# Optimization experiments

Measured on AMD Instinct MI355X. Metric: run time of the kernel, lower is better.

## Reference

```python
import jax, jax.numpy as jnp
import numpy as np

N_NODES = 50000
N_EDGES = 600000
IN_DIM, HID, OUT_DIM = 128, 128, 64


def setup_inputs() -> dict:
    key = jax.random.key(0)
    ks = jax.random.split(key, 12)
    h = jax.random.normal(ks[0], (N_NODES, IN_DIM), dtype=jnp.float32)
    src = jax.random.randint(ks[1], (N_EDGES,), 0, N_NODES, dtype=jnp.int32)
    dst = jax.random.randint(ks[2], (N_EDGES,), 0, N_NODES, dtype=jnp.int32)
    dims = [(IN_DIM, HID), (HID, HID), (HID, HID), (HID, OUT_DIM)]
    params = {}
    for i, (di, do) in enumerate(dims):
        scale = 1.0 / np.sqrt(di)
        params[f"W{i}"] = jax.random.uniform(ks[3 + i], (di, do), jnp.float32, -scale, scale)
        params[f"b{i}"] = jnp.zeros((do,), jnp.float32)
    return dict(h=h, src=src, dst=dst, **params)


def _gcn_layer(h, W, b, src, dst, norm_src, norm_dst, n_nodes):
    # DGL GraphConv, norm='both': D^{-1/2} A D^{-1/2} (h W) + b
    x = (h * norm_src) @ W              # [N, out]
    agg = jax.ops.segment_sum(x[src], dst, num_segments=n_nodes)
    return agg * norm_dst + b


def reference(h, src, dst, W0, b0, W1, b1, W2, b2, W3, b3):
    n = h.shape[0]
    ones = jnp.ones((src.shape[0],), h.dtype)
    deg_out = jnp.clip(jax.ops.segment_sum(ones, src, num_segments=n), 1.0)
    deg_in = jnp.clip(jax.ops.segment_sum(ones, dst, num_segments=n), 1.0)
    norm_src = (deg_out ** -0.5)[:, None]
    norm_dst = (deg_in ** -0.5)[:, None]
    Ws = [(W0, b0), (W1, b1), (W2, b2), (W3, b3)]
    for i, (W, b) in enumerate(Ws):
        h = _gcn_layer(h, W, b, src, dst, norm_src, norm_dst, n)
        if i != len(Ws) - 1:
            h = jax.nn.relu(h)  # dropout is identity in eval mode
    return h
```

## Files before the change

### kernel.cpp

```cpp
#include <hip/hip_runtime.h>


namespace {

constexpr int NN = 50000;
constexpr int NE = 600000;
constexpr int SCAN_BLK = 256;
constexpr int NBLK = (NN + SCAN_BLK - 1) / SCAN_BLK;
constexpr int EB = (NE + 255) / 256;
constexpr int MFMA_BLOCKS = (NN / 16 + 3) / 4;
constexpr int WCVT_ELEMS = 16384 * 3 + 8192;
constexpr int WCVT_BLOCKS = WCVT_ELEMS / 256;

typedef unsigned short bhalf;
typedef __attribute__((ext_vector_type(8))) short short8v;
typedef __attribute__((ext_vector_type(4))) float f32x4;

__device__ inline float blo(unsigned int v) {
  return __uint_as_float(v << 16);
}
__device__ inline float bhi(unsigned int v) {
  return __uint_as_float(v & 0xFFFF0000u);
}
__device__ inline unsigned int f2b_bits(float f) {
  unsigned int b = __float_as_uint(f);
  return b + 0x7FFFu + ((b >> 16) & 1u);
}
__device__ inline unsigned int pack2(float lo, float hi) {
  return (f2b_bits(lo) >> 16) | (f2b_bits(hi) & 0xFFFF0000u);
}
__device__ inline bhalf f2b(float f) { return (bhalf)(f2b_bits(f) >> 16); }

__global__ __launch_bounds__(256) void wcvt_kernel(
    const float* __restrict__ W0, const float* __restrict__ W1,
    const float* __restrict__ W2, const float* __restrict__ W3,
    bhalf* __restrict__ wt0, bhalf* __restrict__ wt1,
    bhalf* __restrict__ wt2, bhalf* __restrict__ wt3) {
  int flat = blockIdx.x * 256 + threadIdx.x;
  if (flat < 16384) {
    int j = flat >> 7, k = flat & 127;
    wt0[flat] = f2b(W0[k * 128 + j]);
  } else if (flat < 32768) {
    int f = flat - 16384;
    int j = f >> 7, k = f & 127;
    wt1[f] = f2b(W1[k * 128 + j]);
  } else if (flat < 49152) {
    int f = flat - 32768;
    int j = f >> 7, k = f & 127;
    wt2[f] = f2b(W2[k * 128 + j]);
  } else {
    int f = flat - 49152;
    int j = f >> 7, k = f & 127;
    wt3[f] = f2b(W3[k * 64 + j]);
  }
}

__global__ void deg_loc_kernel(const int* __restrict__ src, const int* __restrict__ dst,
                               int* __restrict__ dego, int* __restrict__ degi,
                               int* __restrict__ le) {
  int e = blockIdx.x * blockDim.x + threadIdx.x;
  if (e < NE) {
    atomicAdd(&dego[src[e]], 1);
    le[e] = atomicAdd(&degi[dst[e]], 1);
  }
}

__global__ __launch_bounds__(SCAN_BLK) void scan1_norm(const int* __restrict__ dego,
                                                       const int* __restrict__ degi,
                                                       int* __restrict__ bsum,
                                                       float* __restrict__ ns,
                                                       float* __restrict__ nd) {
  __shared__ int ws[SCAN_BLK / 64];
  int i = blockIdx.x * SCAN_BLK + threadIdx.x;
  int v = 0;
  if (i < NN) {
    int din = degi[i];
    int dout = dego[i];
    v = din;
    int a = dout < 1 ? 1 : dout;
    int b = din < 1 ? 1 : din;
    ns[i] = 1.0f / sqrtf((float)a);
    nd[i] = 1.0f / sqrtf((float)b);
  }
#pragma unroll
  for (int off = 32; off; off >>= 1) v += __shfl_down(v, off, 64);
  int lane = threadIdx.x & 63, w = threadIdx.x >> 6;
  if (lane == 0) ws[w] = v;
  __syncthreads();
  if (threadIdx.x == 0) {
    int s = 0;
#pragma unroll
    for (int k = 0; k < SCAN_BLK / 64; ++k) s += ws[k];
    bsum[blockIdx.x] = s;
  }
}

__global__ __launch_bounds__(SCAN_BLK) void scan23(const int* __restrict__ deg,
                                                   const int* __restrict__ bsum,
                                                   int* __restrict__ rowptr) {
  __shared__ int sb[SCAN_BLK];
  __shared__ int s[SCAN_BLK];
  const int t = threadIdx.x;
  int vb = (t < NBLK) ? bsum[t] : 0;
  sb[t] = vb;
  __syncthreads();
  for (int off = 1; off < SCAN_BLK; off <<= 1) {
    int u = (t >= off) ? sb[t - off] : 0;
    __syncthreads();
    sb[t] += u;
    __syncthreads();
  }
  const int pre = (blockIdx.x == 0) ? 0 : sb[blockIdx.x - 1];
  if (blockIdx.x == NBLK - 1 && t == 0) rowptr[NN] = sb[NBLK - 1];

  int i = blockIdx.x * SCAN_BLK + t;
  int v = (i < NN) ? deg[i] : 0;
  s[t] = v;
  __syncthreads();
  for (int off = 1; off < SCAN_BLK; off <<= 1) {
    int u = (t >= off) ? s[t - off] : 0;
    __syncthreads();
    s[t] += u;
    __syncthreads();
  }
  if (i < NN) rowptr[i] = pre + s[t] - v;
}

__global__ void scatter_kernel(const int* __restrict__ src, const int* __restrict__ dst,
                               const int* __restrict__ le, const int* __restrict__ rowptr,
                               int* __restrict__ col) {
  int e = blockIdx.x * blockDim.x + threadIdx.x;
  if (e < NE) col[rowptr[dst[e]] + le[e]] = src[e];
}

template <int DO, bool USE_NS, typename TH>
__global__ __launch_bounds__(256, 2) void gemm_mfma(const TH* __restrict__ h,
                                                    const bhalf* __restrict__ wt,
                                                    const float* __restrict__ ns,
                                                    bhalf* __restrict__ x) {
  constexpr int CF = DO / 16;
  const int lane = threadIdx.x & 63;
  const int wv = threadIdx.x >> 6;
  const int tile = blockIdx.x * 4 + wv;
  if (tile >= NN / 16) return;
  const int row0 = tile * 16;
  const size_t arow = (size_t)(row0 + (lane & 15)) * 128;
  const int koff = (lane >> 4) * 8;
  const int bcol = lane & 15;

  f32x4 acc[CF];
#pragma unroll
  for (int cf = 0; cf < CF; ++cf) acc[cf] = (f32x4){0.f, 0.f, 0.f, 0.f};

#pragma unroll
  for (int ks = 0; ks < 4; ++ks) {
    const int k0 = ks * 32 + koff;
    short8v av;
    if constexpr (sizeof(TH) == 4) {
      float4 ha = *reinterpret_cast<const float4*>(&h[arow + k0]);
      float4 hb = *reinterpret_cast<const float4*>(&h[arow + k0 + 4]);
      av[0] = (short)f2b(ha.x); av[1] = (short)f2b(ha.y);
      av[2] = (short)f2b(ha.z); av[3] = (short)f2b(ha.w);
      av[4] = (short)f2b(hb.x); av[5] = (short)f2b(hb.y);
      av[6] = (short)f2b(hb.z); av[7] = (short)f2b(hb.w);
    } else {
      av = *reinterpret_cast<const short8v*>(&h[arow + k0]);
    }
#pragma unroll
    for (int cf = 0; cf < CF; ++cf) {
      short8v bv = *reinterpret_cast<const short8v*>(
          &wt[(size_t)(cf * 16 + bcol) * 128 + k0]);
      acc[cf] = __builtin_amdgcn_mfma_f32_16x16x32_bf16(av, bv, acc[cf], 0, 0, 0);
    }
  }

  const int crow = row0 + ((lane >> 4) << 2);
  float nsv[4] = {1.f, 1.f, 1.f, 1.f};
  if constexpr (USE_NS) {
#pragma unroll
    for (int r = 0; r < 4; ++r) nsv[r] = ns[crow + r];
  }
#pragma unroll
  for (int cf = 0; cf < CF; ++cf) {
#pragma unroll
    for (int r = 0; r < 4; ++r) {
      x[(size_t)(crow + r) * DO + cf * 16 + bcol] = f2b(acc[cf][r] * nsv[r]);
    }
  }
}

template <int D, bool RELU, bool NSRC, bool OUTBF>
__global__ __launch_bounds__(256) void gather4_kernel(const bhalf* __restrict__ x,
                                                      const int* __restrict__ rowptr,
                                                      const int* __restrict__ col,
                                                      const float* __restrict__ nd,
                                                      const float* __restrict__ b,
                                                      const float* __restrict__ nsv,
                                                      void* __restrict__ outp) {
  constexpr int LPR = D / 8;
  constexpr int NPW = 64 / LPR;
  const int wid = (blockIdx.x * blockDim.x + threadIdx.x) >> 6;
  if (wid * NPW >= NN) return;
  const int lane = threadIdx.x & 63;
  const int g = lane / LPR;
  const int ci = (lane % LPR) * 8;
  const int n = wid * NPW + g;
  const int beg = rowptr[n];
  const int end = rowptr[n + 1];

  float a[8];
#pragma unroll
  for (int k = 0; k < 8; ++k) a[k] = 0.f;

  for (int e = beg; e < end; e += 4) {
    const bool p1 = e + 1 < end;
    const bool p2 = e + 2 < end;
    const bool p3 = e + 3 < end;
    const int c0 = col[e];
    const int c1 = col[p1 ? e + 1 : e];
    const int c2 = col[p2 ? e + 2 : e];
    const int c3 = col[p3 ? e + 3 : e];
    const float s0 = NSRC ? nsv[c0] : 1.0f;
    const float s1 = p1 ? (NSRC ? nsv[c1] : 1.0f) : 0.0f;
    const float s2 = p2 ? (NSRC ? nsv[c2] : 1.0f) : 0.0f;
    const float s3 = p3 ? (NSRC ? nsv[c3] : 1.0f) : 0.0f;
    const uint4 v0 = *reinterpret_cast<const uint4*>(&x[(size_t)c0 * D + ci]);
    const uint4 v1 = *reinterpret_cast<const uint4*>(&x[(size_t)c1 * D + ci]);
    const uint4 v2 = *reinterpret_cast<const uint4*>(&x[(size_t)c2 * D + ci]);
    const uint4 v3 = *reinterpret_cast<const uint4*>(&x[(size_t)c3 * D + ci]);
    float f0[8], f1[8], f2[8], f3[8];
    f0[0] = blo(v0.x); f0[1] = bhi(v0.x); f0[2] = blo(v0.y); f0[3] = bhi(v0.y);
    f0[4] = blo(v0.z); f0[5] = bhi(v0.z); f0[6] = blo(v0.w); f0[7] = bhi(v0.w);
    f1[0] = blo(v1.x); f1[1] = bhi(v1.x); f1[2] = blo(v1.y); f1[3] = bhi(v1.y);
    f1[4] = blo(v1.z); f1[5] = bhi(v1.z); f1[6] = blo(v1.w); f1[7] = bhi(v1.w);
    f2[0] = blo(v2.x); f2[1] = bhi(v2.x); f2[2] = blo(v2.y); f2[3] = bhi(v2.y);
    f2[4] = blo(v2.z); f2[5] = bhi(v2.z); f2[6] = blo(v2.w); f2[7] = bhi(v2.w);
    f3[0] = blo(v3.x); f3[1] = bhi(v3.x); f3[2] = blo(v3.y); f3[3] = bhi(v3.y);
    f3[4] = blo(v3.z); f3[5] = bhi(v3.z); f3[6] = blo(v3.w); f3[7] = bhi(v3.w);
#pragma unroll
    for (int k = 0; k < 8; ++k) {
      a[k] = fmaf(s0, f0[k], fmaf(s1, f1[k], fmaf(s2, f2[k], fmaf(s3, f3[k], a[k]))));
    }
  }

  const float s = nd[n];
  float4 b0 = *reinterpret_cast<const float4*>(&b[ci]);
  float4 b1 = *reinterpret_cast<const float4*>(&b[ci + 4]);
  float r[8];
  r[0] = fmaf(a[0], s, b0.x); r[1] = fmaf(a[1], s, b0.y);
  r[2] = fmaf(a[2], s, b0.z); r[3] = fmaf(a[3], s, b0.w);
  r[4] = fmaf(a[4], s, b1.x); r[5] = fmaf(a[5], s, b1.y);
  r[6] = fmaf(a[6], s, b1.z); r[7] = fmaf(a[7], s, b1.w);
  if (RELU) {
#pragma unroll
    for (int k = 0; k < 8; ++k) r[k] = fmaxf(r[k], 0.f);
  }
  if constexpr (OUTBF) {
    bhalf* out = (bhalf*)outp;
    uint4 p;
    p.x = pack2(r[0], r[1]);
    p.y = pack2(r[2], r[3]);
    p.z = pack2(r[4], r[5]);
    p.w = pack2(r[6], r[7]);
    *reinterpret_cast<uint4*>(&out[(size_t)n * D + ci]) = p;
  } else {
    float* out = (float*)outp;
    *reinterpret_cast<float4*>(&out[(size_t)n * D + ci]) =
        make_float4(r[0], r[1], r[2], r[3]);
    *reinterpret_cast<float4*>(&out[(size_t)n * D + ci + 4]) =
        make_float4(r[4], r[5], r[6], r[7]);
  }
}

}

extern "C" void kernel_launch(void* const* d_in, const int* in_sizes, int n_in,
                              void* d_out, int out_size, void* d_ws, size_t ws_size,
                              hipStream_t stream) {
  const float* h0  = (const float*)d_in[0];
  const int*   src = (const int*)d_in[1];
  const int*   dst = (const int*)d_in[2];
  const float* W0 = (const float*)d_in[3];
  const float* b0 = (const float*)d_in[4];
  const float* W1 = (const float*)d_in[5];
  const float* b1 = (const float*)d_in[6];
  const float* W2 = (const float*)d_in[7];
  const float* b2 = (const float*)d_in[8];
  const float* W3 = (const float*)d_in[9];
  const float* b3 = (const float*)d_in[10];
  float* out = (float*)d_out;

  char* w = (char*)d_ws;
  size_t off = 0;
  auto take = [&](size_t bytes) {
    char* p = w + off;
    off = (off + bytes + 255) & ~size_t(255);
    return p;
  };
  int*   deg_out = (int*)take(NN * 4);
  int*   deg_in  = (int*)take(NN * 4);
  float* nsrc    = (float*)take(NN * 4);
  float* ndst    = (float*)take(NN * 4);
  int*   rowptr  = (int*)take((NN + 1) * 4);
  int*   le      = (int*)take(NE * 4);
  int*   col     = (int*)take(NE * 4);
  int*   bsum    = (int*)take(NBLK * 4);
  bhalf* xbuf    = (bhalf*)take((size_t)NN * 128 * 2);
  bhalf* hbuf    = (bhalf*)take((size_t)NN * 128 * 2);
  bhalf* wt0     = (bhalf*)take(128 * 128 * 2);
  bhalf* wt1     = (bhalf*)take(128 * 128 * 2);
  bhalf* wt2     = (bhalf*)take(128 * 128 * 2);
  bhalf* wt3     = (bhalf*)take(64 * 128 * 2);
  (void)ws_size; (void)in_sizes; (void)n_in; (void)out_size;

  hipMemsetAsync(deg_out, 0, (size_t)((char*)nsrc - (char*)deg_out), stream);

  wcvt_kernel<<<WCVT_BLOCKS, 256, 0, stream>>>(W0, W1, W2, W3, wt0, wt1, wt2, wt3);
  gemm_mfma<128, false, float><<<MFMA_BLOCKS, 256, 0, stream>>>(h0, wt0, nullptr, xbuf);
  deg_loc_kernel<<<EB, 256, 0, stream>>>(src, dst, deg_out, deg_in, le);
  scan1_norm<<<NBLK, SCAN_BLK, 0, stream>>>(deg_out, deg_in, bsum, nsrc, ndst);
  scan23<<<NBLK, SCAN_BLK, 0, stream>>>(deg_in, bsum, rowptr);
  scatter_kernel<<<EB, 256, 0, stream>>>(src, dst, le, rowptr, col);

  const int G4_128 = (NN / 4 * 64) / 256;
  const int G4_64  = (NN / 8 * 64 + 255) / 256;

  gather4_kernel<128, true, true, true><<<G4_128, 256, 0, stream>>>(
      xbuf, rowptr, col, ndst, b0, nsrc, hbuf);
  gemm_mfma<128, true, bhalf><<<MFMA_BLOCKS, 256, 0, stream>>>(hbuf, wt1, nsrc, xbuf);
  gather4_kernel<128, true, false, true><<<G4_128, 256, 0, stream>>>(
      xbuf, rowptr, col, ndst, b1, nullptr, hbuf);
  gemm_mfma<128, true, bhalf><<<MFMA_BLOCKS, 256, 0, stream>>>(hbuf, wt2, nsrc, xbuf);
  gather4_kernel<128, true, false, true><<<G4_128, 256, 0, stream>>>(
      xbuf, rowptr, col, ndst, b2, nullptr, hbuf);
  gemm_mfma<64, true, bhalf><<<MFMA_BLOCKS, 256, 0, stream>>>(hbuf, wt3, nsrc, xbuf);
  gather4_kernel<64, false, false, false><<<G4_64, 256, 0, stream>>>(
      xbuf, rowptr, col, ndst, b3, nullptr, out);
}
```

Measured before the change: 250.2 us.

## Merge independent setup kernels via block-range dispatch to cut launches

Combines the degree-counting atomics with the weight conversion in one launch, and the first scan/norm pass with the layer-0 GEMM in another, picking the role by block index. The two removed launches and their serialization gaps are the target, and the independent work can now overlap on the GPU. The cost is that the fused scan/GEMM kernel runs under launch_bounds(256,2) with the GEMM's register pressure, which may change occupancy for the scan blocks.

```diff
diff --git a/kernel.cpp b/kernel.cpp
--- a/kernel.cpp
+++ b/kernel.cpp
@@ -31,12 +31,22 @@
 }
 __device__ inline bhalf f2b(float f) { return (bhalf)(f2b_bits(f) >> 16); }
 
-__global__ __launch_bounds__(256) void wcvt_kernel(
-    const float* __restrict__ W0, const float* __restrict__ W1,
-    const float* __restrict__ W2, const float* __restrict__ W3,
-    bhalf* __restrict__ wt0, bhalf* __restrict__ wt1,
-    bhalf* __restrict__ wt2, bhalf* __restrict__ wt3) {
-  int flat = blockIdx.x * 256 + threadIdx.x;
+__global__ void deg_wcvt_kernel(const int* __restrict__ src, const int* __restrict__ dst,
+                                int* __restrict__ dego, int* __restrict__ degi,
+                                int* __restrict__ le,
+                                const float* __restrict__ W0, const float* __restrict__ W1,
+                                const float* __restrict__ W2, const float* __restrict__ W3,
+                                bhalf* __restrict__ wt0, bhalf* __restrict__ wt1,
+                                bhalf* __restrict__ wt2, bhalf* __restrict__ wt3) {
+  if (blockIdx.x < EB) {
+    int e = blockIdx.x * blockDim.x + threadIdx.x;
+    if (e < NE) {
+      atomicAdd(&dego[src[e]], 1);
+      le[e] = atomicAdd(&degi[dst[e]], 1);
+    }
+    return;
+  }
+  int flat = (blockIdx.x - EB) * 256 + threadIdx.x;
   if (flat < 16384) {
     int j = flat >> 7, k = flat & 127;
     wt0[flat] = f2b(W0[k * 128 + j]);
@@ -55,21 +65,69 @@
   }
 }
 
-__global__ void deg_loc_kernel(const int* __restrict__ src, const int* __restrict__ dst,
-                               int* __restrict__ dego, int* __restrict__ degi,
-                               int* __restrict__ le) {
-  int e = blockIdx.x * blockDim.x + threadIdx.x;
-  if (e < NE) {
-    atomicAdd(&dego[src[e]], 1);
-    le[e] = atomicAdd(&degi[dst[e]], 1);
-  }
-}
-
-__global__ __launch_bounds__(SCAN_BLK) void scan1_norm(const int* __restrict__ dego,
-                                                       const int* __restrict__ degi,
-                                                       int* __restrict__ bsum,
-                                                       float* __restrict__ ns,
-                                                       float* __restrict__ nd) {
+template <int DO, bool USE_NS, typename TH>
+__device__ void gemm_mfma_body(const TH* __restrict__ h, const bhalf* __restrict__ wt,
+                               const float* __restrict__ ns, bhalf* __restrict__ x,
+                               int tile) {
+  constexpr int CF = DO / 16;
+  const int lane = threadIdx.x & 63;
+  const int row0 = tile * 16;
+  const size_t arow = (size_t)(row0 + (lane & 15)) * 128;
+  const int koff = (lane >> 4) * 8;
+  const int bcol = lane & 15;
+
+  f32x4 acc[CF];
+#pragma unroll
+  for (int cf = 0; cf < CF; ++cf) acc[cf] = (f32x4){0.f, 0.f, 0.f, 0.f};
+
+#pragma unroll
+  for (int ks = 0; ks < 4; ++ks) {
+    const int k0 = ks * 32 + koff;
+    short8v av;
+    if constexpr (sizeof(TH) == 4) {
+      float4 ha = *reinterpret_cast<const float4*>(&h[arow + k0]);
+      float4 hb = *reinterpret_cast<const float4*>(&h[arow + k0 + 4]);
+      av[0] = (short)f2b(ha.x); av[1] = (short)f2b(ha.y);
+      av[2] = (short)f2b(ha.z); av[3] = (short)f2b(ha.w);
+      av[4] = (short)f2b(hb.x); av[5] = (short)f2b(hb.y);
+      av[6] = (short)f2b(hb.z); av[7] = (short)f2b(hb.w);
+    } else {
+      av = *reinterpret_cast<const short8v*>(&h[arow + k0]);
+    }
+#pragma unroll
+    for (int cf = 0; cf < CF; ++cf) {
+      short8v bv = *reinterpret_cast<const short8v*>(
+          &wt[(size_t)(cf * 16 + bcol) * 128 + k0]);
+      acc[cf] = __builtin_amdgcn_mfma_f32_16x16x32_bf16(av, bv, acc[cf], 0, 0, 0);
+    }
+  }
+
+  const int crow = row0 + ((lane >> 4) << 2);
+  float nsv[4] = {1.f, 1.f, 1.f, 1.f};
+  if constexpr (USE_NS) {
+#pragma unroll
+    for (int r = 0; r < 4; ++r) nsv[r] = ns[crow + r];
+  }
+#pragma unroll
+  for (int cf = 0; cf < CF; ++cf) {
+#pragma unroll
+    for (int r = 0; r < 4; ++r) {
+      x[(size_t)(crow + r) * DO + cf * 16 + bcol] = f2b(acc[cf][r] * nsv[r]);
+    }
+  }
+}
+
+__global__ __launch_bounds__(256, 2) void scan1_gemm0_kernel(
+    const int* __restrict__ dego, const int* __restrict__ degi,
+    int* __restrict__ bsum, float* __restrict__ ns, float* __restrict__ nd,
+    const float* __restrict__ h0, const bhalf* __restrict__ wt0,
+    bhalf* __restrict__ x) {
+  if (blockIdx.x >= NBLK) {
+    const int tile = (blockIdx.x - NBLK) * 4 + (threadIdx.x >> 6);
+    if (tile < NN / 16)
+      gemm_mfma_body<128, false, float>(h0, wt0, nullptr, x, tile);
+    return;
+  }
   __shared__ int ws[SCAN_BLK / 64];
   int i = blockIdx.x * SCAN_BLK + threadIdx.x;
   int v = 0;
@@ -138,55 +196,9 @@
                                                     const bhalf* __restrict__ wt,
                                                     const float* __restrict__ ns,
                                                     bhalf* __restrict__ x) {
-  constexpr int CF = DO / 16;
-  const int lane = threadIdx.x & 63;
-  const int wv = threadIdx.x >> 6;
-  const int tile = blockIdx.x * 4 + wv;
+  const int tile = blockIdx.x * 4 + (threadIdx.x >> 6);
   if (tile >= NN / 16) return;
-  const int row0 = tile * 16;
-  const size_t arow = (size_t)(row0 + (lane & 15)) * 128;
-  const int koff = (lane >> 4) * 8;
-  const int bcol = lane & 15;
-
-  f32x4 acc[CF];
-#pragma unroll
-  for (int cf = 0; cf < CF; ++cf) acc[cf] = (f32x4){0.f, 0.f, 0.f, 0.f};
-
-#pragma unroll
-  for (int ks = 0; ks < 4; ++ks) {
-    const int k0 = ks * 32 + koff;
-    short8v av;
-    if constexpr (sizeof(TH) == 4) {
-      float4 ha = *reinterpret_cast<const float4*>(&h[arow + k0]);
-      float4 hb = *reinterpret_cast<const float4*>(&h[arow + k0 + 4]);
-      av[0] = (short)f2b(ha.x); av[1] = (short)f2b(ha.y);
-      av[2] = (short)f2b(ha.z); av[3] = (short)f2b(ha.w);
-      av[4] = (short)f2b(hb.x); av[5] = (short)f2b(hb.y);
-      av[6] = (short)f2b(hb.z); av[7] = (short)f2b(hb.w);
-    } else {
-      av = *reinterpret_cast<const short8v*>(&h[arow + k0]);
-    }
-#pragma unroll
-    for (int cf = 0; cf < CF; ++cf) {
-      short8v bv = *reinterpret_cast<const short8v*>(
-          &wt[(size_t)(cf * 16 + bcol) * 128 + k0]);
-      acc[cf] = __builtin_amdgcn_mfma_f32_16x16x32_bf16(av, bv, acc[cf], 0, 0, 0);
-    }
-  }
-
-  const int crow = row0 + ((lane >> 4) << 2);
-  float nsv[4] = {1.f, 1.f, 1.f, 1.f};
-  if constexpr (USE_NS) {
-#pragma unroll
-    for (int r = 0; r < 4; ++r) nsv[r] = ns[crow + r];
-  }
-#pragma unroll
-  for (int cf = 0; cf < CF; ++cf) {
-#pragma unroll
-    for (int r = 0; r < 4; ++r) {
-      x[(size_t)(crow + r) * DO + cf * 16 + bcol] = f2b(acc[cf][r] * nsv[r]);
-    }
-  }
+  gemm_mfma_body<DO, USE_NS, TH>(h, wt, ns, x, tile);
 }
 
 template <int D, bool RELU, bool NSRC, bool OUTBF>
@@ -315,10 +327,10 @@
 
   hipMemsetAsync(deg_out, 0, (size_t)((char*)nsrc - (char*)deg_out), stream);
 
-  wcvt_kernel<<<WCVT_BLOCKS, 256, 0, stream>>>(W0, W1, W2, W3, wt0, wt1, wt2, wt3);
-  gemm_mfma<128, false, float><<<MFMA_BLOCKS, 256, 0, stream>>>(h0, wt0, nullptr, xbuf);
-  deg_loc_kernel<<<EB, 256, 0, stream>>>(src, dst, deg_out, deg_in, le);
-  scan1_norm<<<NBLK, SCAN_BLK, 0, stream>>>(deg_out, deg_in, bsum, nsrc, ndst);
+  deg_wcvt_kernel<<<EB + WCVT_BLOCKS, 256, 0, stream>>>(
+      src, dst, deg_out, deg_in, le, W0, W1, W2, W3, wt0, wt1, wt2, wt3);
+  scan1_gemm0_kernel<<<NBLK + MFMA_BLOCKS, 256, 0, stream>>>(
+      deg_out, deg_in, bsum, nsrc, ndst, h0, wt0, xbuf);
   scan23<<<NBLK, SCAN_BLK, 0, stream>>>(deg_in, bsum, rowptr);
   scatter_kernel<<<EB, 256, 0, stream>>>(src, dst, le, rowptr, col);
 
```

New measurement: 248.0 us. No clear change (-0.9%).
